# Performance work log

Hardware: AMD Instinct MI355X
Metric: run time of the kernel (lower is better)

Reference implementation:

```python
import jax, jax.numpy as jnp
import numpy as np

EPS = 1e-12  # matches torch F.normalize eps

def _l2norm(x, axis):
    n = jnp.sqrt(jnp.sum(x * x, axis=axis, keepdims=True))
    return x / jnp.maximum(n, EPS)

def setup_inputs() -> dict:
    key = jax.random.key(0)
    b, N, c, h, w = 8, 4, 256, 64, 64
    n, hw, L = N - 1, h * w, 2048
    k1, k2, k3, k4, k5 = jax.random.split(key, 5)
    feat = jax.random.normal(k1, (b, c, h, w), dtype=jnp.float32)
    refs = jax.random.normal(k2, (b, N, c, h, w), dtype=jnp.float32)
    similarity = jax.random.uniform(k3, (b, N), dtype=jnp.float32)
    # unique indices per row (the torch code pads by repeating mask indices; we use
    # unique ones so the final scatter is deterministic)
    base_indices = jax.vmap(lambda k: jax.random.permutation(k, hw))(jax.random.split(k4, b))[:, :L].astype(jnp.int64)
    ref_idx = jax.vmap(lambda k: jax.random.permutation(k, hw))(jax.random.split(k5, b * n))
    ref_indices_in = ref_idx.reshape(b, n, hw)[:, :, :L].astype(jnp.int64)
    return {"feat": feat, "refs": refs, "similarity": similarity,
            "base_indices": base_indices, "ref_indices_in": ref_indices_in, "index": 0}

def reference(feat, refs, similarity, base_indices, ref_indices_in, index):
    b, N, c, h, w = refs.shape
    n, hw = N - 1, h * w
    L = base_indices.shape[1]
    # drop the base reference slot
    refs_r = jnp.concatenate([refs[:, :index], refs[:, index + 1:]], axis=1)      # [b,n,c,h,w]
    base_sim = similarity[:, index]                                              # [b]
    ref_sims = jnp.concatenate([similarity[:, :index], similarity[:, index + 1:]], axis=1)  # [b,n]

    feat_flat = feat.reshape(b, c, hw)                                           # [b,c,hw]
    w_feat = _l2norm(feat_flat.transpose(0, 2, 1), axis=2)                       # [b,hw,c]
    w_refs = _l2norm(refs_r.reshape(b, n, c, hw), axis=2)                        # [b,n,c,hw]

    # gather masked positions
    feat_select = jnp.take_along_axis(feat_flat, base_indices[:, None, :], axis=2)      # [b,c,L]
    w_feat_sel = _l2norm(jnp.take_along_axis(w_feat, base_indices[:, :, None], axis=1), axis=2)  # [b,L,c]
    w_ref_sel = jnp.take_along_axis(w_refs, ref_indices_in[:, :, None, :], axis=3)      # [b,n,c,L]

    # cosine similarity + top-1 match per base position, per reference
    fx = jnp.einsum('blc,bncm->bnlm', w_feat_sel, w_ref_sel)                     # [b,n,L,L]
    ref_indices = jnp.argmax(fx, axis=3)                                         # [b,n,L] (top-1)
    ref_selects = jnp.take_along_axis(w_ref_sel, ref_indices[:, :, None, :], axis=3)    # [b,n,c,L]

    # similarity-weighted fusion
    feat_fused = base_sim[:, None, None] * feat_select \
               + jnp.einsum('bn,bncl->bcl', ref_sims, ref_selects)               # [b,c,L]

    # scatter fused features back into the base feature map
    bi = jnp.arange(b)[:, None, None]
    ci = jnp.arange(c)[None, :, None]
    out = feat_flat.at[bi, ci, base_indices[:, None, :]].set(feat_fused)
    return out.reshape(b, c, h, w), base_indices, ref_indices
```

## Files before the change

kernel.cpp:

```cpp
#include <hip/hip_runtime.h>
#include <math.h>

#define HWp 4096
#define Cp 256
#define Lp 2048
#define Np 3
#define Bp 8

#define OUT_FEAT_N 8388608
#define OUT_BASE_OFF 8388608
#define OUT_REF_OFF 8404992
#define NROWS 49152

#define OFF_AT    ((size_t)0)
#define OFF_BT    ((size_t)16777216)
#define OFF_BF16  ((size_t)67108864)
#define OFF_PVAL  ((size_t)117440512)
#define OFF_BEST  ((size_t)119799808)
#define OFF_CAND2 ((size_t)119996416)
#define OFF_COUNT ((size_t)120193024)
#define OFF_LIST  ((size_t)120193280)
#define OFF_INV   ((size_t)120389888)

typedef _Float16 f16x8 __attribute__((ext_vector_type(8)));
typedef float f32x4 __attribute__((ext_vector_type(4)));

__device__ __forceinline__ unsigned short f16bits(float x){
    union { _Float16 h; unsigned short s; } u;
    u.h = (_Float16)x;
    return u.s;
}

__global__ void init_inv_kernel(int4* __restrict__ inv4){
    int tid = blockIdx.x * blockDim.x + threadIdx.x;
    if (tid < 32768) inv4[tid] = make_int4(-1, -1, -1, -1);
}

__global__ void scatter_inv_kernel(const int* __restrict__ refIdxI,
                                   const int* __restrict__ baseIdx,
                                   int* __restrict__ inv){
    int tid = blockIdx.x * blockDim.x + threadIdx.x;
    if (tid < NROWS){
        int g = tid >> 11;
        inv[g*4096 + refIdxI[tid]] = tid & 2047;
    } else if (tid < NROWS + Bp*Lp){
        int t = tid - NROWS;
        int b = t >> 11;
        inv[(24 + b)*4096 + baseIdx[t]] = t & 2047;
    }
}

__global__ __launch_bounds__(256) void gather_kernel(
    const float* __restrict__ feat, const float* __restrict__ refs,
    const int* __restrict__ pindex, const int* __restrict__ inv,
    float* __restrict__ A_T, float* __restrict__ B_T,
    unsigned char* __restrict__ Bf16)
{
    int tileh = blockIdx.x & 127;
    int g = blockIdx.x >> 7;
    int isRef = (g < 24);
    const float* src;
    int b;
    if (isRef){
        b = g / 3; int r0 = g - b*3; int iv = *pindex;
        int rn = (r0 < iv) ? r0 : r0 + 1;
        src = refs + ((size_t)(b*4 + rn)) * Cp * HWp;
    } else {
        b = g - 24;
        src = feat + (size_t)b * Cp * HWp;
    }
    __shared__ float lds[32 * 256];
    int tid = threadIdx.x, hwl = tid & 31, cg = tid >> 5;
    int hw0 = tileh * 32;
    const float* sp = src + hw0 + hwl;
    int swz = (hwl & 7) << 3;
    float* lrow = lds + hwl * 256;
    #pragma unroll
    for (int i = 0; i < 8; i++){
        int c0 = cg * 32 + i * 4;
        float x0 = sp[(size_t)(c0 + 0) * HWp];
        float x1 = sp[(size_t)(c0 + 1) * HWp];
        float x2 = sp[(size_t)(c0 + 2) * HWp];
        float x3 = sp[(size_t)(c0 + 3) * HWp];
        *(float4*)(lrow + (c0 ^ swz)) = make_float4(x0, x1, x2, x3);
    }
    __syncthreads();
    int w = tid >> 6, lane = tid & 63;
    const int* invg = inv + g * 4096 + hw0;
    for (int h = w * 8; h < w * 8 + 8; h++){
        int dest = invg[h];
        if (dest < 0) continue;
        float4 v = *(float4*)(lds + h * 256 + ((lane * 4) ^ ((h & 7) << 3)));
        float ssq = v.x*v.x + v.y*v.y + v.z*v.z + v.w*v.w;
        #pragma unroll
        for (int off = 1; off < 64; off <<= 1) ssq += __shfl_xor(ssq, off, 64);
        float dn = fmaxf(sqrtf(ssq), 1e-12f);
        v.x /= dn; v.y /= dn; v.z /= dn; v.w /= dn;
        if (isRef){
            size_t row = ((size_t)g * Lp + dest) * Cp;
            *(float4*)(B_T + row + lane * 4) = v;
            ushort4 hv;
            hv.x = f16bits(v.x); hv.y = f16bits(v.y);
            hv.z = f16bits(v.z); hv.w = f16bits(v.w);
            *(ushort4*)(Bf16 + ((size_t)g * Lp + dest) * 512 + lane * 8) = hv;
        } else {
            size_t row = ((size_t)b * Lp + dest) * Cp;
            *(float4*)(A_T + row + lane * 4) = v;
        }
    }
}

__device__ __forceinline__ void stage4(const unsigned char* srcLane, unsigned char* ldsW){
    #pragma unroll
    for (int p = 0; p < 4; p++)
        __builtin_amdgcn_global_load_lds(
            (const __attribute__((address_space(1))) void*)(srcLane + (p & 1) * 8192 + (p >> 1) * 64),
            (__attribute__((address_space(3))) void*)(ldsW + p * 1024),
            16, 0, 0);
}

__global__ __launch_bounds__(256, 3) void gemm_mfma_kernel(
    const float* __restrict__ A_T, const unsigned char* __restrict__ Bf16,
    unsigned int* __restrict__ ppk)
{
    int orig = (blockIdx.x & 7) * 192 + (blockIdx.x >> 3);
    int rowgrp = orig & 15;
    int chunk = (orig >> 4) % 12;
    int b = orig / 192;
    int n = chunk >> 2, c4 = chunk & 3;
    int bn = b*3 + n;
    int tid = threadIdx.x, lane = tid & 63, w = tid >> 6;
    int l15 = lane & 15, lg = lane >> 4;

    __shared__ unsigned char bufs[2][16384];

    int row0 = rowgrp*128 + w*16 + l15;
    const float* Arow0 = A_T + ((size_t)b*Lp + row0)*Cp + lg*8;
    const float* Arow1 = Arow0 + (size_t)64*Cp;
    union U8 { _Float16 h[8]; f16x8 v; };
    U8 A0[8], A1[8];
    #pragma unroll
    for (int ks = 0; ks < 8; ks++){
        float4 fa = *(const float4*)(Arow0 + ks*32);
        float4 fb = *(const float4*)(Arow0 + ks*32 + 4);
        float xs[8] = {fa.x, fa.y, fa.z, fa.w, fb.x, fb.y, fb.z, fb.w};
        #pragma unroll
        for (int jj = 0; jj < 8; jj++) A0[ks].h[jj] = (_Float16)xs[jj];
        float4 fc = *(const float4*)(Arow1 + ks*32);
        float4 fd = *(const float4*)(Arow1 + ks*32 + 4);
        float ys[8] = {fc.x, fc.y, fc.z, fc.w, fd.x, fd.y, fd.z, fd.w};
        #pragma unroll
        for (int jj = 0; jj < 8; jj++) A1[ks].h[jj] = (_Float16)ys[jj];
    }

    unsigned p1[8], p2[8];
    #pragma unroll
    for (int s = 0; s < 8; s++){ p1[s] = 0u; p2[s] = 0u; }

    const unsigned char* srcLane = Bf16
        + ((size_t)(bn*2048 + c4*512)) * 512
        + l15 * 512 + (lane >> 4) * 16 + w * 128;
    unsigned char* ldsW0 = &bufs[0][w*4096];
    unsigned char* ldsW1 = &bufs[1][w*4096];

    stage4(srcLane, ldsW0);

    #pragma unroll 1
    for (int t = 0; t < 16; t++){
        if (t < 15){
            stage4(srcLane + (size_t)(t+1)*16384, (t & 1) ? ldsW0 : ldsW1);
            asm volatile("s_waitcnt vmcnt(4)" ::: "memory");
        } else {
            asm volatile("s_waitcnt vmcnt(0)" ::: "memory");
        }
        __builtin_amdgcn_s_barrier();

        const unsigned char* bp = bufs[t & 1];
        f32x4 a00 = {2.f,2.f,2.f,2.f}, a01 = {2.f,2.f,2.f,2.f};
        f32x4 a10 = {2.f,2.f,2.f,2.f}, a11 = {2.f,2.f,2.f,2.f};
        #pragma unroll
        for (int ks = 0; ks < 8; ks++){
            f16x8 b0 = *(const f16x8*)(bp + ks*2048 + lane*16);
            f16x8 b1 = *(const f16x8*)(bp + ks*2048 + 1024 + lane*16);
            a00 = __builtin_amdgcn_mfma_f32_16x16x32_f16(A0[ks].v, b0, a00, 0, 0, 0);
            a01 = __builtin_amdgcn_mfma_f32_16x16x32_f16(A0[ks].v, b1, a01, 0, 0, 0);
            a10 = __builtin_amdgcn_mfma_f32_16x16x32_f16(A1[ks].v, b0, a10, 0, 0, 0);
            a11 = __builtin_amdgcn_mfma_f32_16x16x32_f16(A1[ks].v, b1, a11, 0, 0, 0);
        }
        __builtin_amdgcn_s_barrier();

        unsigned ci0 = (unsigned)(511 - (t*32 + l15));
        unsigned ci1 = ci0 - 16;
        #pragma unroll
        for (int r = 0; r < 4; r++){
            {
                unsigned u0 = (__float_as_uint(a00[r]) & 0xFFFFFE00u) | ci0;
                unsigned u1 = (__float_as_uint(a01[r]) & 0xFFFFFE00u) | ci1;
                unsigned hi = max(u0, u1), lo = min(u0, u1);
                unsigned tm = min(p1[r], hi);
                p1[r] = max(p1[r], hi);
                p2[r] = max(p2[r], max(lo, tm));
            }
            {
                unsigned u0 = (__float_as_uint(a10[r]) & 0xFFFFFE00u) | ci0;
                unsigned u1 = (__float_as_uint(a11[r]) & 0xFFFFFE00u) | ci1;
                unsigned hi = max(u0, u1), lo = min(u0, u1);
                unsigned tm = min(p1[4+r], hi);
                p1[4+r] = max(p1[4+r], hi);
                p2[4+r] = max(p2[4+r], max(lo, tm));
            }
        }
    }

    #pragma unroll
    for (int s = 0; s < 8; s++){
        unsigned q1 = p1[s], q2 = p2[s];
        #pragma unroll
        for (int off = 1; off < 16; off <<= 1){
            unsigned o1 = (unsigned)__shfl_xor((int)q1, off, 64);
            unsigned o2 = (unsigned)__shfl_xor((int)q2, off, 64);
            unsigned m1 = max(q1, o1);
            unsigned m2 = max(min(q1, o1), max(q2, o2));
            q1 = m1; q2 = m2;
        }
        if (l15 == 0){
            int rs = s >> 2, r = s & 3;
            size_t grow = (size_t)bn*Lp + rowgrp*128 + rs*64 + w*16 + lg*4 + r;
            size_t slot = grow*4 + c4;
            ppk[slot*2 + 0] = q1;
            ppk[slot*2 + 1] = q2;
        }
    }
}

__global__ void reset_kernel(int* count){ *count = 0; }

__global__ void combine_kernel(const unsigned int* __restrict__ ppk,
                               int* __restrict__ best, int* __restrict__ cand2,
                               float* __restrict__ outF, const int* __restrict__ baseIdx,
                               int* __restrict__ count, int* __restrict__ list)
{
    int gid = blockIdx.x * blockDim.x + threadIdx.x;
    if (gid < NROWS){
        unsigned V1 = 0u, V2 = 0u; int X1 = 0, X2 = 0;
        #pragma unroll
        for (int ch = 0; ch < 4; ch++){
            unsigned u1 = ppk[((size_t)gid*4 + ch)*2 + 0];
            unsigned u2 = ppk[((size_t)gid*4 + ch)*2 + 1];
            unsigned vb1 = u1 & 0xFFFFFE00u; int c1 = ch*512 + 511 - (int)(u1 & 511u);
            unsigned vb2 = u2 & 0xFFFFFE00u; int c2 = ch*512 + 511 - (int)(u2 & 511u);
            if (vb1 > V1 || (vb1 == V1 && c1 < X1)){
                V2 = V1; X2 = X1; V1 = vb1; X1 = c1;
            } else if (vb1 > V2 || (vb1 == V2 && c1 < X2)){
                V2 = vb1; X2 = c1;
            }
            if (vb2 > V2 || (vb2 == V2 && c2 < X2)){ V2 = vb2; X2 = c2; }
        }
        best[gid] = X1; cand2[gid] = X2;
        outF[OUT_REF_OFF + gid] = (float)X1;
        if (__uint_as_float(V1) - __uint_as_float(V2) < 3.6e-4f){
            int s = atomicAdd(count, 1);
            if (s < NROWS) list[s] = gid;
        }
    }
    if (gid < Bp*Lp) outF[OUT_BASE_OFF + gid] = (float)baseIdx[gid];
}

__global__ void refine_kernel(const float* __restrict__ A_T, const float* __restrict__ B_T,
                              const int* __restrict__ count, const int* __restrict__ list,
                              int* __restrict__ best, const int* __restrict__ cand2,
                              float* __restrict__ outF)
{
    int nf = *count; if (nf > NROWS) nf = NROWS;
    int lane = threadIdx.x & 63;
    for (int it = blockIdx.x; it < nf; it += gridDim.x){
        int gid = list[it];
        int bn = gid >> 11, l = gid & 2047;
        int b = bn / 3;
        int i1 = best[gid], i2 = cand2[gid];
        const float* ar  = A_T + ((size_t)b*Lp + l) * Cp;
        const float* b1r = B_T + ((size_t)bn*Lp + i1) * Cp;
        const float* b2r = B_T + ((size_t)bn*Lp + i2) * Cp;
        double d1 = 0.0, d2 = 0.0;
        #pragma unroll
        for (int j = 0; j < 4; j++){
            double a = (double)ar[lane*4 + j];
            d1 += a * (double)b1r[lane*4 + j];
            d2 += a * (double)b2r[lane*4 + j];
        }
        #pragma unroll
        for (int off = 1; off < 64; off <<= 1){
            d1 += __shfl_xor(d1, off, 64);
            d2 += __shfl_xor(d2, off, 64);
        }
        if (lane == 0){
            int ix = (d2 > d1 || (d2 == d1 && i2 < i1)) ? i2 : i1;
            best[gid] = ix;
            outF[OUT_REF_OFF + gid] = (float)ix;
        }
    }
}

__global__ __launch_bounds__(256) void fuse_tile_kernel(
    const float* __restrict__ feat, const float* __restrict__ B_T,
    const int* __restrict__ best, const int* __restrict__ inv,
    const float* __restrict__ sim, const int* __restrict__ pindex,
    float* __restrict__ out)
{
    int tileh = blockIdx.x & 63;
    int b = blockIdx.x >> 6;
    int hw0 = tileh * 64;
    __shared__ float lds[256 * 64];
    int tid = threadIdx.x, hwl = tid & 63, cg = tid >> 6;
    const float* fb = feat + (size_t)b * Cp * HWp + hw0 + hwl;
    #pragma unroll 4
    for (int i = 0; i < 64; i++){
        int c = cg * 64 + i;
        lds[c * 64 + ((hwl + c) & 63)] = fb[(size_t)c * HWp];
    }
    __syncthreads();
    int iv = *pindex;
    float bs  = sim[b*4 + iv];
    float rs0 = sim[b*4 + ((0 < iv) ? 0 : 1)];
    float rs1 = sim[b*4 + ((1 < iv) ? 1 : 2)];
    float rs2 = sim[b*4 + ((2 < iv) ? 2 : 3)];
    int w = cg, lane = tid & 63;
    const int* invg = inv + (24 + b) * 4096 + hw0;
    for (int h = w * 16; h < w * 16 + 16; h++){
        int dest = invg[h];
        if (dest < 0) continue;
        int b0 = best[(b*3 + 0)*Lp + dest];
        int b1 = best[(b*3 + 1)*Lp + dest];
        int b2 = best[(b*3 + 2)*Lp + dest];
        const float* r0 = B_T + ((size_t)(b*3 + 0)*Lp + b0) * Cp;
        const float* r1 = B_T + ((size_t)(b*3 + 1)*Lp + b1) * Cp;
        const float* r2 = B_T + ((size_t)(b*3 + 2)*Lp + b2) * Cp;
        #pragma unroll
        for (int j = 0; j < 4; j++){
            int c = lane + j * 64;
            int la = c * 64 + ((h + c) & 63);
            float base = lds[la];
            lds[la] = bs*base + rs0*r0[c] + rs1*r1[c] + rs2*r2[c];
        }
    }
    __syncthreads();
    float* ob = out + (size_t)b * Cp * HWp + hw0 + hwl;
    #pragma unroll 4
    for (int i = 0; i < 64; i++){
        int c = cg * 64 + i;
        ob[(size_t)c * HWp] = lds[c * 64 + ((hwl + c) & 63)];
    }
}

extern "C" void kernel_launch(void* const* d_in, const int* in_sizes, int n_in,
                              void* d_out, int out_size, void* d_ws, size_t ws_size,
                              hipStream_t stream)
{
    const float* feat    = (const float*)d_in[0];
    const float* refs    = (const float*)d_in[1];
    const float* sim     = (const float*)d_in[2];
    const int*   baseIdx = (const int*)d_in[3];
    const int*   refIdxI = (const int*)d_in[4];
    const int*   pindex  = (const int*)d_in[5];
    float* out = (float*)d_out;
    unsigned char* ws = (unsigned char*)d_ws;

    float* A_T   = (float*)(ws + OFF_AT);
    float* B_T   = (float*)(ws + OFF_BT);
    unsigned char* Bf16 = ws + OFF_BF16;
    unsigned int* ppk = (unsigned int*)(ws + OFF_PVAL);
    int* best  = (int*)(ws + OFF_BEST);
    int* cand2 = (int*)(ws + OFF_CAND2);
    int* count = (int*)(ws + OFF_COUNT);
    int* list  = (int*)(ws + OFF_LIST);
    int* inv   = (int*)(ws + OFF_INV);

    init_inv_kernel<<<128, 256, 0, stream>>>((int4*)inv);
    scatter_inv_kernel<<<256, 256, 0, stream>>>(refIdxI, baseIdx, inv);
    gather_kernel<<<4096, 256, 0, stream>>>(feat, refs, pindex, inv, A_T, B_T, Bf16);
    gemm_mfma_kernel<<<1536, 256, 0, stream>>>(A_T, Bf16, ppk);
    reset_kernel<<<1, 1, 0, stream>>>(count);
    combine_kernel<<<192, 256, 0, stream>>>(ppk, best, cand2, out, baseIdx, count, list);
    refine_kernel<<<512, 64, 0, stream>>>(A_T, B_T, count, list, best, cand2, out);
    fuse_tile_kernel<<<512, 256, 0, stream>>>(feat, B_T, best, inv, sim, pindex, out);
}
```

Measured before the change: 167.3 us.

## Drop fp32 normalized intermediates and keep only fp16 gathered copies

The gather kernel now writes only fp16 normalized rows, for both the base features and the references, instead of fp32 A_T/B_T plus an fp16 B copy. The GEMM loads fp16 A operands directly and no longer converts them, and the fuse kernel reads fp16 reference rows. The refine kernel recomputes exact dot products and norms in double precision from the original strided feat/refs tensors. This removes a large volume of workspace writes and reads. In exchange, refine does uncoalesced channel-strided reads, and the fused output values carry fp16 rounding error that may approach tolerance limits.

```diff
diff --git a/kernel.cpp b/kernel.cpp
--- a/kernel.cpp
+++ b/kernel.cpp
@@ -12,9 +12,8 @@
 #define OUT_REF_OFF 8404992
 #define NROWS 49152
 
-#define OFF_AT    ((size_t)0)
-#define OFF_BT    ((size_t)16777216)
-#define OFF_BF16  ((size_t)67108864)
+#define OFF_AF16  ((size_t)0)
+#define OFF_BF16  ((size_t)16777216)
 #define OFF_PVAL  ((size_t)117440512)
 #define OFF_BEST  ((size_t)119799808)
 #define OFF_CAND2 ((size_t)119996416)
@@ -53,8 +52,7 @@
 __global__ __launch_bounds__(256) void gather_kernel(
     const float* __restrict__ feat, const float* __restrict__ refs,
     const int* __restrict__ pindex, const int* __restrict__ inv,
-    float* __restrict__ A_T, float* __restrict__ B_T,
-    unsigned char* __restrict__ Bf16)
+    unsigned char* __restrict__ Af16, unsigned char* __restrict__ Bf16)
 {
     int tileh = blockIdx.x & 127;
     int g = blockIdx.x >> 7;
@@ -87,6 +85,8 @@
     __syncthreads();
     int w = tid >> 6, lane = tid & 63;
     const int* invg = inv + g * 4096 + hw0;
+    unsigned char* dstBase = isRef ? (Bf16 + (size_t)g * Lp * 512)
+                                   : (Af16 + (size_t)b * Lp * 512);
     for (int h = w * 8; h < w * 8 + 8; h++){
         int dest = invg[h];
         if (dest < 0) continue;
@@ -96,17 +96,10 @@
         for (int off = 1; off < 64; off <<= 1) ssq += __shfl_xor(ssq, off, 64);
         float dn = fmaxf(sqrtf(ssq), 1e-12f);
         v.x /= dn; v.y /= dn; v.z /= dn; v.w /= dn;
-        if (isRef){
-            size_t row = ((size_t)g * Lp + dest) * Cp;
-            *(float4*)(B_T + row + lane * 4) = v;
-            ushort4 hv;
-            hv.x = f16bits(v.x); hv.y = f16bits(v.y);
-            hv.z = f16bits(v.z); hv.w = f16bits(v.w);
-            *(ushort4*)(Bf16 + ((size_t)g * Lp + dest) * 512 + lane * 8) = hv;
-        } else {
-            size_t row = ((size_t)b * Lp + dest) * Cp;
-            *(float4*)(A_T + row + lane * 4) = v;
-        }
+        ushort4 hv;
+        hv.x = f16bits(v.x); hv.y = f16bits(v.y);
+        hv.z = f16bits(v.z); hv.w = f16bits(v.w);
+        *(ushort4*)(dstBase + (size_t)dest * 512 + lane * 8) = hv;
     }
 }
 
@@ -120,7 +113,7 @@
 }
 
 __global__ __launch_bounds__(256, 3) void gemm_mfma_kernel(
-    const float* __restrict__ A_T, const unsigned char* __restrict__ Bf16,
+    const unsigned char* __restrict__ Af16, const unsigned char* __restrict__ Bf16,
     unsigned int* __restrict__ ppk)
 {
     int orig = (blockIdx.x & 7) * 192 + (blockIdx.x >> 3);
@@ -135,22 +128,13 @@
     __shared__ unsigned char bufs[2][16384];
 
     int row0 = rowgrp*128 + w*16 + l15;
-    const float* Arow0 = A_T + ((size_t)b*Lp + row0)*Cp + lg*8;
-    const float* Arow1 = Arow0 + (size_t)64*Cp;
-    union U8 { _Float16 h[8]; f16x8 v; };
-    U8 A0[8], A1[8];
+    const unsigned char* Arow0 = Af16 + ((size_t)b*Lp + row0)*512 + lg*16;
+    const unsigned char* Arow1 = Arow0 + (size_t)64*512;
+    f16x8 A0[8], A1[8];
     #pragma unroll
     for (int ks = 0; ks < 8; ks++){
-        float4 fa = *(const float4*)(Arow0 + ks*32);
-        float4 fb = *(const float4*)(Arow0 + ks*32 + 4);
-        float xs[8] = {fa.x, fa.y, fa.z, fa.w, fb.x, fb.y, fb.z, fb.w};
-        #pragma unroll
-        for (int jj = 0; jj < 8; jj++) A0[ks].h[jj] = (_Float16)xs[jj];
-        float4 fc = *(const float4*)(Arow1 + ks*32);
-        float4 fd = *(const float4*)(Arow1 + ks*32 + 4);
-        float ys[8] = {fc.x, fc.y, fc.z, fc.w, fd.x, fd.y, fd.z, fd.w};
-        #pragma unroll
-        for (int jj = 0; jj < 8; jj++) A1[ks].h[jj] = (_Float16)ys[jj];
+        A0[ks] = *(const f16x8*)(Arow0 + ks*64);
+        A1[ks] = *(const f16x8*)(Arow1 + ks*64);
     }
 
     unsigned p1[8], p2[8];
@@ -182,10 +166,10 @@
         for (int ks = 0; ks < 8; ks++){
             f16x8 b0 = *(const f16x8*)(bp + ks*2048 + lane*16);
             f16x8 b1 = *(const f16x8*)(bp + ks*2048 + 1024 + lane*16);
-            a00 = __builtin_amdgcn_mfma_f32_16x16x32_f16(A0[ks].v, b0, a00, 0, 0, 0);
-            a01 = __builtin_amdgcn_mfma_f32_16x16x32_f16(A0[ks].v, b1, a01, 0, 0, 0);
-            a10 = __builtin_amdgcn_mfma_f32_16x16x32_f16(A1[ks].v, b0, a10, 0, 0, 0);
-            a11 = __builtin_amdgcn_mfma_f32_16x16x32_f16(A1[ks].v, b1, a11, 0, 0, 0);
+            a00 = __builtin_amdgcn_mfma_f32_16x16x32_f16(A0[ks], b0, a00, 0, 0, 0);
+            a01 = __builtin_amdgcn_mfma_f32_16x16x32_f16(A0[ks], b1, a01, 0, 0, 0);
+            a10 = __builtin_amdgcn_mfma_f32_16x16x32_f16(A1[ks], b0, a10, 0, 0, 0);
+            a11 = __builtin_amdgcn_mfma_f32_16x16x32_f16(A1[ks], b1, a11, 0, 0, 0);
         }
         __builtin_amdgcn_s_barrier();
 
@@ -266,35 +250,49 @@
     if (gid < Bp*Lp) outF[OUT_BASE_OFF + gid] = (float)baseIdx[gid];
 }
 
-__global__ void refine_kernel(const float* __restrict__ A_T, const float* __restrict__ B_T,
+__global__ void refine_kernel(const float* __restrict__ feat, const float* __restrict__ refs,
+                              const int* __restrict__ baseIdx, const int* __restrict__ refIdxI,
+                              const int* __restrict__ pindex,
                               const int* __restrict__ count, const int* __restrict__ list,
                               int* __restrict__ best, const int* __restrict__ cand2,
                               float* __restrict__ outF)
 {
     int nf = *count; if (nf > NROWS) nf = NROWS;
     int lane = threadIdx.x & 63;
+    int iv = *pindex;
     for (int it = blockIdx.x; it < nf; it += gridDim.x){
         int gid = list[it];
         int bn = gid >> 11, l = gid & 2047;
-        int b = bn / 3;
+        int b = bn / 3; int r0 = bn - b*3;
+        int rn = (r0 < iv) ? r0 : r0 + 1;
         int i1 = best[gid], i2 = cand2[gid];
-        const float* ar  = A_T + ((size_t)b*Lp + l) * Cp;
-        const float* b1r = B_T + ((size_t)bn*Lp + i1) * Cp;
-        const float* b2r = B_T + ((size_t)bn*Lp + i2) * Cp;
-        double d1 = 0.0, d2 = 0.0;
+        int posA = baseIdx[b*Lp + l];
+        int pos1 = refIdxI[bn*Lp + i1];
+        int pos2 = refIdxI[bn*Lp + i2];
+        const float* fA = feat + (size_t)b * Cp * HWp + posA;
+        const float* fR = refs + (size_t)(b*4 + rn) * Cp * HWp;
+        const float* f1 = fR + pos1;
+        const float* f2 = fR + pos2;
+        double s1 = 0, s2 = 0, d1 = 0, d2 = 0;
         #pragma unroll
         for (int j = 0; j < 4; j++){
-            double a = (double)ar[lane*4 + j];
-            d1 += a * (double)b1r[lane*4 + j];
-            d2 += a * (double)b2r[lane*4 + j];
+            int c = lane * 4 + j;
+            double a  = (double)fA[(size_t)c * HWp];
+            double x1 = (double)f1[(size_t)c * HWp];
+            double x2 = (double)f2[(size_t)c * HWp];
+            s1 += x1*x1; s2 += x2*x2;
+            d1 += a*x1;  d2 += a*x2;
         }
         #pragma unroll
         for (int off = 1; off < 64; off <<= 1){
+            s1 += __shfl_xor(s1, off, 64);
+            s2 += __shfl_xor(s2, off, 64);
             d1 += __shfl_xor(d1, off, 64);
             d2 += __shfl_xor(d2, off, 64);
         }
         if (lane == 0){
-            int ix = (d2 > d1 || (d2 == d1 && i2 < i1)) ? i2 : i1;
+            double q1 = d1 * sqrt(s2), q2 = d2 * sqrt(s1);
+            int ix = (q2 > q1 || (q2 == q1 && i2 < i1)) ? i2 : i1;
             best[gid] = ix;
             outF[OUT_REF_OFF + gid] = (float)ix;
         }
@@ -302,7 +300,7 @@
 }
 
 __global__ __launch_bounds__(256) void fuse_tile_kernel(
-    const float* __restrict__ feat, const float* __restrict__ B_T,
+    const float* __restrict__ feat, const unsigned char* __restrict__ Bf16,
     const int* __restrict__ best, const int* __restrict__ inv,
     const float* __restrict__ sim, const int* __restrict__ pindex,
     float* __restrict__ out)
@@ -332,15 +330,18 @@
         int b0 = best[(b*3 + 0)*Lp + dest];
         int b1 = best[(b*3 + 1)*Lp + dest];
         int b2 = best[(b*3 + 2)*Lp + dest];
-        const float* r0 = B_T + ((size_t)(b*3 + 0)*Lp + b0) * Cp;
-        const float* r1 = B_T + ((size_t)(b*3 + 1)*Lp + b1) * Cp;
-        const float* r2 = B_T + ((size_t)(b*3 + 2)*Lp + b2) * Cp;
+        const unsigned char* r0 = Bf16 + ((size_t)(b*3 + 0)*Lp + b0) * 512;
+        const unsigned char* r1 = Bf16 + ((size_t)(b*3 + 1)*Lp + b1) * 512;
+        const unsigned char* r2 = Bf16 + ((size_t)(b*3 + 2)*Lp + b2) * 512;
         #pragma unroll
         for (int j = 0; j < 4; j++){
             int c = lane + j * 64;
             int la = c * 64 + ((h + c) & 63);
             float base = lds[la];
-            lds[la] = bs*base + rs0*r0[c] + rs1*r1[c] + rs2*r2[c];
+            float v0 = (float)(*(const _Float16*)(r0 + c*2));
+            float v1 = (float)(*(const _Float16*)(r1 + c*2));
+            float v2 = (float)(*(const _Float16*)(r2 + c*2));
+            lds[la] = bs*base + rs0*v0 + rs1*v1 + rs2*v2;
         }
     }
     __syncthreads();
@@ -365,8 +366,7 @@
     float* out = (float*)d_out;
     unsigned char* ws = (unsigned char*)d_ws;
 
-    float* A_T   = (float*)(ws + OFF_AT);
-    float* B_T   = (float*)(ws + OFF_BT);
+    unsigned char* Af16 = ws + OFF_AF16;
     unsigned char* Bf16 = ws + OFF_BF16;
     unsigned int* ppk = (unsigned int*)(ws + OFF_PVAL);
     int* best  = (int*)(ws + OFF_BEST);
@@ -377,10 +377,10 @@
 
     init_inv_kernel<<<128, 256, 0, stream>>>((int4*)inv);
     scatter_inv_kernel<<<256, 256, 0, stream>>>(refIdxI, baseIdx, inv);
-    gather_kernel<<<4096, 256, 0, stream>>>(feat, refs, pindex, inv, A_T, B_T, Bf16);
-    gemm_mfma_kernel<<<1536, 256, 0, stream>>>(A_T, Bf16, ppk);
+    gather_kernel<<<4096, 256, 0, stream>>>(feat, refs, pindex, inv, Af16, Bf16);
+    gemm_mfma_kernel<<<1536, 256, 0, stream>>>(Af16, Bf16, ppk);
     reset_kernel<<<1, 1, 0, stream>>>(count);
     combine_kernel<<<192, 256, 0, stream>>>(ppk, best, cand2, out, baseIdx, count, list);
-    refine_kernel<<<512, 64, 0, stream>>>(A_T, B_T, count, list, best, cand2, out);
-    fuse_tile_kernel<<<512, 256, 0, stream>>>(feat, B_T, best, inv, sim, pindex, out);
-}
+    refine_kernel<<<512, 64, 0, stream>>>(feat, refs, baseIdx, refIdxI, pindex, count, list, best, cand2, out);
+    fuse_tile_kernel<<<512, 256, 0, stream>>>(feat, Bf16, best, inv, sim, pindex, out);
+}
```

Result: faster. 158.8 us (-5.1%).
